# Optimization experiments

Hardware: AMD Instinct MI355X
Metric: run time of the kernel (lower is better)

## Reference

```python
import jax, jax.numpy as jnp
import numpy as np

B, N, S, D_IN, D_OUT = 8, 8192, 8, 64, 64


def setup_inputs() -> dict:
    key = jax.random.key(0)
    ks = jax.random.split(key, 7)
    x = jax.random.normal(ks[0], (B, N, D_IN), dtype=jnp.float32)
    j_idx = jax.random.randint(ks[1], (B, N, S), 0, N, dtype=jnp.int32)
    k_idx = jax.random.randint(ks[2], (B, N, S), 0, N, dtype=jnp.int32)
    # MLP params: Linear(3d -> 2d), GELU, Linear(2d -> d_out)
    s1 = 1.0 / np.sqrt(3 * D_IN)
    s2 = 1.0 / np.sqrt(2 * D_IN)
    W1 = jax.random.uniform(ks[3], (3 * D_IN, 2 * D_IN), jnp.float32, -s1, s1)
    b1 = jax.random.uniform(ks[4], (2 * D_IN,), jnp.float32, -s1, s1)
    W2 = jax.random.uniform(ks[5], (2 * D_IN, D_OUT), jnp.float32, -s2, s2)
    b2 = jax.random.uniform(ks[6], (D_OUT,), jnp.float32, -s2, s2)
    return {"x": x, "j_idx": j_idx, "k_idx": k_idx, "W1": W1, "b1": b1, "W2": W2, "b2": b2}


def reference(x, j_idx, k_idx, W1, b1, W2, b2):
    # x: (B,N,D); j_idx/k_idx: (B,N,S) indices into N
    gather = jax.vmap(lambda xb, ib: xb[ib])  # per-batch gather -> (N,S,D)
    xj = gather(x, j_idx)                      # (B,N,S,D)
    xk = gather(x, k_idx)                      # (B,N,S,D)
    xi = jnp.broadcast_to(x[:, :, None, :], xj.shape)
    triple = jnp.concatenate([xi, xj, xk], axis=-1)  # (B,N,S,3D)
    h = jax.nn.gelu(triple @ W1 + b1, approximate=False)  # (B,N,S,2D)
    out = h @ W2 + b2                                       # (B,N,S,D_OUT)
    return out.mean(axis=2)                                 # (B,N,D_OUT)
```

## Files before the change

kernel.cpp:

```cpp
#include <hip/hip_runtime.h>
#include <stdint.h>


typedef short  short8 __attribute__((ext_vector_type(8)));
typedef float  f32x2  __attribute__((ext_vector_type(2)));
typedef float  f32x4  __attribute__((ext_vector_type(4)));
typedef float  f32x16 __attribute__((ext_vector_type(16)));
typedef _Float16 h16x2 __attribute__((ext_vector_type(2)));

__device__ __forceinline__ unsigned short f2bf(float f){
  union { float f; unsigned u; } a; a.f = f;
  unsigned u = a.u;
  u += 0x7fffu + ((u >> 16) & 1u);
  return (unsigned short)(u >> 16);
}
__device__ __forceinline__ f32x2 gelu2(f32x2 x){
  f32x2 x2 = x * x;
  f32x2 t  = x2 * (-0.1029437f) + (-2.3022083f);
  f32x2 xt = x * t;
  f32x2 r;
  r[0] = __builtin_amdgcn_rcpf(1.0f + __builtin_amdgcn_exp2f(xt[0]));
  r[1] = __builtin_amdgcn_rcpf(1.0f + __builtin_amdgcn_exp2f(xt[1]));
  return x * r;
}

__global__ void prep_w(const float* __restrict__ W1, const float* __restrict__ W2,
                       short* __restrict__ w1f, short* __restrict__ w2f){
  int t0 = threadIdx.x;
  for (int c = t0; c < 48 * 64; c += 256){
    int lane = c & 63, f = c >> 6;
    int cb = f >> 2, t = f & 3;
    short8 v;
    #pragma unroll
    for (int j = 0; j < 8; j++)
      v[j] = (short)f2bf(W1[((cb >> 2) * 64 + t * 16 + 8 * (lane >> 5) + j) * 128
                            + (cb & 3) * 32 + (lane & 31)]);
    *(short8*)(w1f + (long)c * 8) = v;
  }
  for (int c = t0; c < 16 * 64; c += 256){
    int lane = c & 63, g = c >> 6;
    int w = g >> 2, q = g & 3;
    short8 v;
    #pragma unroll
    for (int j = 0; j < 8; j++)
      v[j] = (short)f2bf(W2[(q * 32 + 8 * (lane >> 4) + j) * 64 + w * 16 + (lane & 15)]);
    *(short8*)(w2f + (long)c * 8) = v;
  }
}

__global__ __launch_bounds__(256, 4) void pgemm(
    const float* __restrict__ x, const short* __restrict__ w1f,
    const float* __restrict__ b1, _Float16* __restrict__ P)
{
  const int tid = threadIdx.x;
  const int w = tid >> 6, lane = tid & 63;
  const int l31 = lane & 31, hi = lane >> 5;
  const int bid = blockIdx.x;
  const int n0 = (bid & 7) * 8192 + (bid >> 3) * 32;

  short8 af[4];
  #pragma unroll
  for (int t = 0; t < 4; t++){
    const float* xr = x + (long)(n0 + l31) * 64 + t * 16 + 8 * hi;
    float4 a = *(const float4*)xr;
    float4 b = *(const float4*)(xr + 4);
    short8 v;
    v[0]=(short)f2bf(a.x); v[1]=(short)f2bf(a.y); v[2]=(short)f2bf(a.z); v[3]=(short)f2bf(a.w);
    v[4]=(short)f2bf(b.x); v[5]=(short)f2bf(b.y); v[6]=(short)f2bf(b.z); v[7]=(short)f2bf(b.w);
    af[t] = v;
  }

  #pragma unroll
  for (int ci = 0; ci < 3; ci++){
    const int cb = w * 3 + ci;
    float binit = (cb < 4) ? b1[cb * 32 + l31] : 0.0f;
    f32x16 acc;
    #pragma unroll
    for (int r = 0; r < 16; r++) acc[r] = binit;
    #pragma unroll
    for (int t = 0; t < 4; t++){
      short8 bf = *(const short8*)(w1f + (long)((cb * 4 + t) * 64 + lane) * 8);
      acc = __builtin_amdgcn_mfma_f32_32x32x16_bf16(af[t], bf, acc, 0, 0, 0);
    }
    _Float16* pb = P + (long)n0 * 384 + cb * 32 + l31;
    #pragma unroll
    for (int r = 0; r < 16; r++){
      int row = (r & 3) + 8 * (r >> 2) + 4 * hi;
      pb[(long)row * 384] = (_Float16)acc[r];
    }
  }
}

#define NT2 8
__global__ __launch_bounds__(256, 4) void ltc_main(
    const _Float16* __restrict__ P, const short* __restrict__ w2f,
    const int* __restrict__ jidx,   const int* __restrict__ kidx,
    const float* __restrict__ b2,   float* __restrict__ out)
{
  __shared__ short HB[2][8 * 136];

  const int tid  = threadIdx.x;
  const int w    = tid >> 6, lane = tid & 63;
  const int l15  = lane & 15, q4 = lane >> 4;

  short8 w2v[4];
  #pragma unroll
  for (int q = 0; q < 4; q++)
    w2v[q] = *(const short8*)(w2f + (long)((w * 4 + q) * 64 + lane) * 8);
  const float b2v = b2[w * 16 + l15];

  const int bid   = blockIdx.x;
  const int batch = bid & 7;
  const int gbase = batch * 8192 + (bid >> 3) * 64;
  const unsigned bb = (unsigned)(batch << 13);

  auto gemm2_store = [&](int hb, int ttp){
    f32x4 acc2 = {0.f, 0.f, 0.f, 0.f};
    #pragma unroll
    for (int q2 = 0; q2 < 4; q2++){
      short8 hbf = *(const short8*)((const char*)&HB[hb][0] + (l15 & 7) * 272 + q2 * 64 + q4 * 16);
      acc2 = __builtin_amdgcn_mfma_f32_16x16x32_bf16(hbf, w2v[q2], acc2, 0, 0, 0);
    }
    if (lane < 32){
      long NG = (long)(gbase + ttp * 8);
      #pragma unroll
      for (int r = 0; r < 4; r++)
        out[(NG + 4 * q4 + r) * 64 + w * 16 + l15] = acc2[r] + b2v;
    }
  };

  for (int tt = 0; tt < NT2; ++tt){
    asm volatile("s_waitcnt lgkmcnt(0)\n\ts_barrier" ::: "memory");
    if (tt > 0) gemm2_store((tt ^ 1) & 1, tt - 1);

    #pragma unroll
    for (int u = 0; u < 2; u++){
      const int nn = tt * 8 + w * 2 + u;
      const int gn = gbase + nn;
      const int4* jp = (const int4*)(jidx + (long)gn * 8);
      const int4* kp = (const int4*)(kidx + (long)gn * 8);
      int4 j0 = jp[0], j1 = jp[1];
      int4 k0 = kp[0], k1 = kp[1];
      int jv[8] = {j0.x, j0.y, j0.z, j0.w, j1.x, j1.y, j1.z, j1.w};
      int kv[8] = {k0.x, k0.y, k0.z, k0.w, k1.x, k1.y, k1.z, k1.w};

      h16x2 av = *(const h16x2*)((const char*)P + (unsigned)gn * 768u + lane * 4u);
      f32x2 af; af[0] = (float)av[0]; af[1] = (float)av[1];

      f32x2 hs = {0.f, 0.f};
      #pragma unroll
      for (int s = 0; s < 8; s++){
        unsigned o1 = (bb + (unsigned)jv[s]) * 768u + 256u + lane * 4u;
        unsigned o2 = (bb + (unsigned)kv[s]) * 768u + 512u + lane * 4u;
        h16x2 v1 = *(const h16x2*)((const char*)P + o1);
        h16x2 v2 = *(const h16x2*)((const char*)P + o2);
        f32x2 z;
        z[0] = af[0] + (float)v1[0] + (float)v2[0];
        z[1] = af[1] + (float)v1[1] + (float)v2[1];
        hs += gelu2(z);
      }
      hs *= 0.125f;
      unsigned pk = (unsigned)f2bf(hs[0]) | ((unsigned)f2bf(hs[1]) << 16);
      *(unsigned*)&HB[tt & 1][(w * 2 + u) * 136 + lane * 2] = pk;
    }
  }

  asm volatile("s_waitcnt lgkmcnt(0)\n\ts_barrier" ::: "memory");
  gemm2_store((NT2 - 1) & 1, NT2 - 1);
}

__global__ void ltc_naive(const float* __restrict__ x, const int* __restrict__ jidx,
                          const int* __restrict__ kidx, const float* __restrict__ W1,
                          const float* __restrict__ b1, const float* __restrict__ W2,
                          const float* __restrict__ b2, float* __restrict__ out)
{
  int gidx = blockIdx.x;
  int b = gidx >> 13;
  __shared__ float trip[8][192];
  __shared__ float hb[128];
  int t = threadIdx.x;
  for (int i = t; i < 8 * 192; i += 128){
    int s = i / 192, c = i - s * 192;
    int v = c >> 6, cc = c & 63;
    int src;
    if (v == 0)      src = gidx & 8191;
    else if (v == 1) src = jidx[gidx * 8 + s];
    else             src = kidx[gidx * 8 + s];
    trip[s][c] = x[((long)(b << 13) + src) * 64 + cc];
  }
  __syncthreads();
  float z[8];
  #pragma unroll
  for (int s = 0; s < 8; s++) z[s] = b1[t];
  for (int k = 0; k < 192; k++){
    float wv = W1[k * 128 + t];
    #pragma unroll
    for (int s = 0; s < 8; s++) z[s] = fmaf(trip[s][k], wv, z[s]);
  }
  float acc = 0.f;
  #pragma unroll
  for (int s = 0; s < 8; s++){
    f32x2 zz; zz[0] = z[s]; zz[1] = z[s];
    acc += gelu2(zz)[0];
  }
  hb[t] = acc * 0.125f;
  __syncthreads();
  if (t < 64){
    float o = b2[t];
    for (int h = 0; h < 128; h++) o = fmaf(hb[h], W2[h * 64 + t], o);
    out[(long)gidx * 64 + t] = o;
  }
}

extern "C" void kernel_launch(void* const* d_in, const int* in_sizes, int n_in,
                              void* d_out, int out_size, void* d_ws, size_t ws_size,
                              hipStream_t stream) {
  const float* x   = (const float*)d_in[0];
  const int*   jix = (const int*)  d_in[1];
  const int*   kix = (const int*)  d_in[2];
  const float* W1  = (const float*)d_in[3];
  const float* b1  = (const float*)d_in[4];
  const float* W2  = (const float*)d_in[5];
  const float* b2  = (const float*)d_in[6];
  float* out = (float*)d_out;

  const size_t w1f_elems = 48 * 64 * 8;
  const size_t w2f_elems = 16 * 64 * 8;
  const size_t p_elems   = (size_t)65536 * 384;
  const size_t need = (w1f_elems + w2f_elems + p_elems) * 2;

  if (ws_size >= need){
    short*    w1f = (short*)d_ws;
    short*    w2f = w1f + w1f_elems;
    _Float16* P   = (_Float16*)(w2f + w2f_elems);
    prep_w<<<1, 256, 0, stream>>>(W1, W2, w1f, w2f);
    pgemm<<<2048, 256, 0, stream>>>(x, w1f, b1, P);
    ltc_main<<<1024, 256, 0, stream>>>(P, w2f, jix, kix, b2, out);
  } else {
    ltc_naive<<<8 * 8192, 128, 0, stream>>>(x, jix, kix, W1, b1, W2, b2, out);
  }
}
```

Before: 65.46 us.

## Split projection buffer into self and gather arrays, vectorize stores, widen gemm2 tiles

Splits the per-node projection buffer into a 128-wide self part and a 256-wide gathered part so that the j and k gathers hit a denser array. pgemm swaps the MFMA operands so each lane writes packed 4-half vectors instead of strided scalar stores. The bias b1 is now added in the main kernel rather than folded into the accumulator. ltc_main processes 16 nodes per tile so all 64 lanes of the second GEMM produce useful output, and it sums the two gathered halves in fp16 before widening, which costs some precision. prep_w is spread across 64 blocks instead of running in one block.

```diff
diff --git a/kernel.cpp b/kernel.cpp
--- a/kernel.cpp
+++ b/kernel.cpp
@@ -7,6 +7,7 @@
 typedef float  f32x4  __attribute__((ext_vector_type(4)));
 typedef float  f32x16 __attribute__((ext_vector_type(16)));
 typedef _Float16 h16x2 __attribute__((ext_vector_type(2)));
+typedef _Float16 h16x4 __attribute__((ext_vector_type(4)));
 
 __device__ __forceinline__ unsigned short f2bf(float f){
   union { float f; unsigned u; } a; a.f = f;
@@ -26,31 +27,27 @@
 
 __global__ void prep_w(const float* __restrict__ W1, const float* __restrict__ W2,
                        short* __restrict__ w1f, short* __restrict__ w2f){
-  int t0 = threadIdx.x;
-  for (int c = t0; c < 48 * 64; c += 256){
-    int lane = c & 63, f = c >> 6;
-    int cb = f >> 2, t = f & 3;
-    short8 v;
+  const int f = blockIdx.x, lane = threadIdx.x;
+  short8 v;
+  if (f < 48){
+    const int cb = f >> 2, t = f & 3;
     #pragma unroll
     for (int j = 0; j < 8; j++)
       v[j] = (short)f2bf(W1[((cb >> 2) * 64 + t * 16 + 8 * (lane >> 5) + j) * 128
                             + (cb & 3) * 32 + (lane & 31)]);
-    *(short8*)(w1f + (long)c * 8) = v;
-  }
-  for (int c = t0; c < 16 * 64; c += 256){
-    int lane = c & 63, g = c >> 6;
-    int w = g >> 2, q = g & 3;
-    short8 v;
+    *(short8*)(w1f + (long)(f * 64 + lane) * 8) = v;
+  } else {
+    const int g = f - 48, w = g >> 2, q = g & 3;
     #pragma unroll
     for (int j = 0; j < 8; j++)
       v[j] = (short)f2bf(W2[(q * 32 + 8 * (lane >> 4) + j) * 64 + w * 16 + (lane & 15)]);
-    *(short8*)(w2f + (long)c * 8) = v;
+    *(short8*)(w2f + (long)(g * 64 + lane) * 8) = v;
   }
 }
 
 __global__ __launch_bounds__(256, 4) void pgemm(
     const float* __restrict__ x, const short* __restrict__ w1f,
-    const float* __restrict__ b1, _Float16* __restrict__ P)
+    _Float16* __restrict__ PA, _Float16* __restrict__ PG)
 {
   const int tid = threadIdx.x;
   const int w = tid >> 6, lane = tid & 63;
@@ -58,7 +55,7 @@
   const int bid = blockIdx.x;
   const int n0 = (bid & 7) * 8192 + (bid >> 3) * 32;
 
-  short8 af[4];
+  short8 xf[4];
   #pragma unroll
   for (int t = 0; t < 4; t++){
     const float* xr = x + (long)(n0 + l31) * 64 + t * 16 + 8 * hi;
@@ -67,37 +64,41 @@
     short8 v;
     v[0]=(short)f2bf(a.x); v[1]=(short)f2bf(a.y); v[2]=(short)f2bf(a.z); v[3]=(short)f2bf(a.w);
     v[4]=(short)f2bf(b.x); v[5]=(short)f2bf(b.y); v[6]=(short)f2bf(b.z); v[7]=(short)f2bf(b.w);
-    af[t] = v;
+    xf[t] = v;
   }
 
   #pragma unroll
   for (int ci = 0; ci < 3; ci++){
     const int cb = w * 3 + ci;
-    float binit = (cb < 4) ? b1[cb * 32 + l31] : 0.0f;
     f32x16 acc;
     #pragma unroll
-    for (int r = 0; r < 16; r++) acc[r] = binit;
+    for (int r = 0; r < 16; r++) acc[r] = 0.f;
     #pragma unroll
     for (int t = 0; t < 4; t++){
-      short8 bf = *(const short8*)(w1f + (long)((cb * 4 + t) * 64 + lane) * 8);
-      acc = __builtin_amdgcn_mfma_f32_32x32x16_bf16(af[t], bf, acc, 0, 0, 0);
-    }
-    _Float16* pb = P + (long)n0 * 384 + cb * 32 + l31;
-    #pragma unroll
-    for (int r = 0; r < 16; r++){
-      int row = (r & 3) + 8 * (r >> 2) + 4 * hi;
-      pb[(long)row * 384] = (_Float16)acc[r];
-    }
-  }
-}
-
-#define NT2 8
+      short8 wf = *(const short8*)(w1f + (long)((cb * 4 + t) * 64 + lane) * 8);
+      acc = __builtin_amdgcn_mfma_f32_32x32x16_bf16(wf, xf[t], acc, 0, 0, 0);
+    }
+    _Float16* base = (cb < 4)
+        ? (PA + (long)(n0 + l31) * 128 + cb * 32)
+        : (PG + (long)(n0 + l31) * 256 + (cb - 4) * 32);
+    #pragma unroll
+    for (int g = 0; g < 4; g++){
+      h16x4 pk;
+      pk[0] = (_Float16)acc[4*g+0]; pk[1] = (_Float16)acc[4*g+1];
+      pk[2] = (_Float16)acc[4*g+2]; pk[3] = (_Float16)acc[4*g+3];
+      *(h16x4*)(base + 8 * g + 4 * hi) = pk;
+    }
+  }
+}
+
 __global__ __launch_bounds__(256, 4) void ltc_main(
-    const _Float16* __restrict__ P, const short* __restrict__ w2f,
+    const _Float16* __restrict__ PA, const _Float16* __restrict__ PG,
+    const short* __restrict__ w2f,
     const int* __restrict__ jidx,   const int* __restrict__ kidx,
-    const float* __restrict__ b2,   float* __restrict__ out)
+    const float* __restrict__ b1,   const float* __restrict__ b2,
+    float* __restrict__ out)
 {
-  __shared__ short HB[2][8 * 136];
+  __shared__ short HB[2][16 * 136];
 
   const int tid  = threadIdx.x;
   const int w    = tid >> 6, lane = tid & 63;
@@ -108,6 +109,7 @@
   for (int q = 0; q < 4; q++)
     w2v[q] = *(const short8*)(w2f + (long)((w * 4 + q) * 64 + lane) * 8);
   const float b2v = b2[w * 16 + l15];
+  const float2 b1p = *(const float2*)(b1 + lane * 2);
 
   const int bid   = blockIdx.x;
   const int batch = bid & 7;
@@ -118,55 +120,52 @@
     f32x4 acc2 = {0.f, 0.f, 0.f, 0.f};
     #pragma unroll
     for (int q2 = 0; q2 < 4; q2++){
-      short8 hbf = *(const short8*)((const char*)&HB[hb][0] + (l15 & 7) * 272 + q2 * 64 + q4 * 16);
+      short8 hbf = *(const short8*)((const char*)&HB[hb][0] + l15 * 272 + q2 * 64 + q4 * 16);
       acc2 = __builtin_amdgcn_mfma_f32_16x16x32_bf16(hbf, w2v[q2], acc2, 0, 0, 0);
     }
-    if (lane < 32){
-      long NG = (long)(gbase + ttp * 8);
-      #pragma unroll
-      for (int r = 0; r < 4; r++)
-        out[(NG + 4 * q4 + r) * 64 + w * 16 + l15] = acc2[r] + b2v;
-    }
+    long Gn = (long)(gbase + ttp * 16);
+    #pragma unroll
+    for (int r = 0; r < 4; r++)
+      out[(Gn + 4 * q4 + r) * 64 + w * 16 + l15] = acc2[r] + b2v;
   };
 
-  for (int tt = 0; tt < NT2; ++tt){
+  for (int tt = 0; tt < 4; ++tt){
     asm volatile("s_waitcnt lgkmcnt(0)\n\ts_barrier" ::: "memory");
     if (tt > 0) gemm2_store((tt ^ 1) & 1, tt - 1);
 
     #pragma unroll
-    for (int u = 0; u < 2; u++){
-      const int nn = tt * 8 + w * 2 + u;
-      const int gn = gbase + nn;
-      const int4* jp = (const int4*)(jidx + (long)gn * 8);
-      const int4* kp = (const int4*)(kidx + (long)gn * 8);
-      int4 j0 = jp[0], j1 = jp[1];
-      int4 k0 = kp[0], k1 = kp[1];
-      int jv[8] = {j0.x, j0.y, j0.z, j0.w, j1.x, j1.y, j1.z, j1.w};
-      int kv[8] = {k0.x, k0.y, k0.z, k0.w, k1.x, k1.y, k1.z, k1.w};
-
-      h16x2 av = *(const h16x2*)((const char*)P + (unsigned)gn * 768u + lane * 4u);
-      f32x2 af; af[0] = (float)av[0]; af[1] = (float)av[1];
+    for (int u = 0; u < 4; u++){
+      const int nl = w * 4 + u;
+      const int gn = gbase + tt * 16 + nl;
+      const int4 j0 = *(const int4*)(jidx + (long)gn * 8);
+      const int4 j1 = *(const int4*)(jidx + (long)gn * 8 + 4);
+      const int4 k0 = *(const int4*)(kidx + (long)gn * 8);
+      const int4 k1 = *(const int4*)(kidx + (long)gn * 8 + 4);
+      const int jv[8] = {j0.x, j0.y, j0.z, j0.w, j1.x, j1.y, j1.z, j1.w};
+      const int kv[8] = {k0.x, k0.y, k0.z, k0.w, k1.x, k1.y, k1.z, k1.w};
+
+      h16x2 av = *(const h16x2*)(PA + (long)gn * 128 + lane * 2);
+      f32x2 af; af[0] = (float)av[0] + b1p.x; af[1] = (float)av[1] + b1p.y;
 
       f32x2 hs = {0.f, 0.f};
       #pragma unroll
       for (int s = 0; s < 8; s++){
-        unsigned o1 = (bb + (unsigned)jv[s]) * 768u + 256u + lane * 4u;
-        unsigned o2 = (bb + (unsigned)kv[s]) * 768u + 512u + lane * 4u;
-        h16x2 v1 = *(const h16x2*)((const char*)P + o1);
-        h16x2 v2 = *(const h16x2*)((const char*)P + o2);
+        h16x2 v1 = *(const h16x2*)(PG + (long)(bb + (unsigned)jv[s]) * 256 + lane * 2);
+        h16x2 v2 = *(const h16x2*)(PG + (long)(bb + (unsigned)kv[s]) * 256 + 128 + lane * 2);
+        h16x2 vs = v1 + v2;
         f32x2 z;
-        z[0] = af[0] + (float)v1[0] + (float)v2[0];
-        z[1] = af[1] + (float)v1[1] + (float)v2[1];
+        z[0] = af[0] + (float)vs[0];
+        z[1] = af[1] + (float)vs[1];
         hs += gelu2(z);
       }
       hs *= 0.125f;
       unsigned pk = (unsigned)f2bf(hs[0]) | ((unsigned)f2bf(hs[1]) << 16);
-      *(unsigned*)&HB[tt & 1][(w * 2 + u) * 136 + lane * 2] = pk;
+      *(unsigned*)&HB[tt & 1][nl * 136 + lane * 2] = pk;
     }
   }
 
   asm volatile("s_waitcnt lgkmcnt(0)\n\ts_barrier" ::: "memory");
-  gemm2_store((NT2 - 1) & 1, NT2 - 1);
+  gemm2_store(1, 3);
 }
 
 __global__ void ltc_naive(const float* __restrict__ x, const int* __restrict__ jidx,
@@ -226,16 +225,18 @@
 
   const size_t w1f_elems = 48 * 64 * 8;
   const size_t w2f_elems = 16 * 64 * 8;
-  const size_t p_elems   = (size_t)65536 * 384;
-  const size_t need = (w1f_elems + w2f_elems + p_elems) * 2;
+  const size_t pa_elems  = (size_t)65536 * 128;
+  const size_t pg_elems  = (size_t)65536 * 256;
+  const size_t need = (w1f_elems + w2f_elems + pa_elems + pg_elems) * 2;
 
   if (ws_size >= need){
     short*    w1f = (short*)d_ws;
     short*    w2f = w1f + w1f_elems;
-    _Float16* P   = (_Float16*)(w2f + w2f_elems);
-    prep_w<<<1, 256, 0, stream>>>(W1, W2, w1f, w2f);
-    pgemm<<<2048, 256, 0, stream>>>(x, w1f, b1, P);
-    ltc_main<<<1024, 256, 0, stream>>>(P, w2f, jix, kix, b2, out);
+    _Float16* PA  = (_Float16*)(w2f + w2f_elems);
+    _Float16* PG  = PA + pa_elems;
+    prep_w<<<64, 64, 0, stream>>>(W1, W2, w1f, w2f);
+    pgemm<<<2048, 256, 0, stream>>>(x, w1f, PA, PG);
+    ltc_main<<<1024, 256, 0, stream>>>(PA, PG, w2f, jix, kix, b1, b2, out);
   } else {
     ltc_naive<<<8 * 8192, 128, 0, stream>>>(x, jix, kix, W1, b1, W2, b2, out);
   }
```

Result: slower. 67.83 us (+3.6%).
